# Optimization experiments

Hardware: AMD Instinct MI355X
Metric: run time of the kernel (lower is better)

Reference implementation:

```python
import jax, jax.numpy as jnp
import numpy as np

MIN_CONTEXT_SIZE = 64
FUTURE_STEPS = 12


def setup_inputs() -> dict:
    key = jax.random.key(0)
    k1, k2, k3 = jax.random.split(key, 3)
    B, T, E, C = 32, 256, 256, 256
    embeddings = jax.random.normal(k1, (B, T, E), dtype=jnp.float32)
    contexts = jax.random.normal(k2, (B, T, C), dtype=jnp.float32)
    # Bilinear comparator weight, scaled like a typical linear init
    W = jax.random.normal(k3, (E, C), dtype=jnp.float32) * (1.0 / np.sqrt(E).astype(np.float32))
    return {"embeddings": embeddings, "contexts": contexts, "W": W}


def reference(embeddings, contexts, W):
    B, T, E = embeddings.shape
    log_probs = []
    for step in range(FUTURE_STEPS):
        emb = embeddings[:, MIN_CONTEXT_SIZE + step:T]          # (B, S, E)
        ctx = contexts[:, MIN_CONTEXT_SIZE - 1:T - step - 1]    # (B, S, C)
        S = T - step - MIN_CONTEXT_SIZE
        # all-pairs bilinear scores: score[b,s,j,t] = emb[b,s] @ W @ ctx[j,t]
        proj = jnp.einsum('bse,ec->bsc', emb, W)                # (B, S, C)
        scores = jnp.einsum('bsc,jtc->bsjt', proj, ctx)         # (B, S, B, S)
        flat = scores.reshape(B * S, B * S)
        positives = jnp.diagonal(flat).reshape(B, S)            # matched (b,s) pairs
        lse = jax.nn.logsumexp(scores.reshape(B, S, B * S), axis=-1)
        lse = lse - jnp.log(jnp.asarray(B * S, dtype=scores.dtype))
        log_probs.append((positives - lse).reshape(-1))
    flat_log_probs = jnp.concatenate(log_probs, axis=0)
    return -flat_log_probs.mean()
```

## Files before the change

kernel.cpp:

```cpp
#include <hip/hip_runtime.h>
#include <hip/hip_bf16.h>
#include <math.h>


#define NROW 6144
#define TAIL0 181
#define NTERMS 71616.0f
#define LOG2E 1.44269504088896340736f
#define SHIFT2 92.33248261689366f

typedef __attribute__((ext_vector_type(8))) short short8;
typedef __attribute__((ext_vector_type(4))) float f32x4;

__device__ __forceinline__ ushort f2bf(float f) {
  union { float f; uint32_t u; } v; v.f = f;
  uint32_t u = v.u;
  return (ushort)((u + 0x7FFFu + ((u >> 16) & 1u)) >> 16);
}
__device__ __forceinline__ float expsh(float x) {
  return exp2f(fmaf(x, LOG2E, -SHIFT2));
}

__device__ __forceinline__ void gload16(const ushort* g, ushort* l) {
  __builtin_amdgcn_global_load_lds((const __attribute__((address_space(1))) void*)g,
                                   (__attribute__((address_space(3))) void*)l, 16, 0, 0);
}

__global__ __launch_bounds__(256) void k_cast(const float* __restrict__ ctx,
                                              const float* __restrict__ W,
                                              ushort* __restrict__ X,
                                              ushort* __restrict__ Wt,
                                              float* __restrict__ zbase) {
  int bi = blockIdx.x;
  if (bi < 1536) {
    int idx = bi * 256 + threadIdx.x;
    int row = idx >> 6, f4 = idx & 63;
    int j = row & 31, t = row >> 5;
    float4 f = *(const float4*)(ctx + ((size_t)(j * 256 + 63 + t)) * 256 + f4 * 4);
    ushort4 o;
    o.x = f2bf(f.x); o.y = f2bf(f.y); o.z = f2bf(f.z); o.w = f2bf(f.w);
    ((ushort4*)(X + (size_t)row * 256))[f4] = o;
  } else if (bi < 1792) {
    int c = bi - 1536, e = threadIdx.x;
    Wt[c * 256 + e] = f2bf(W[e * 256 + c]);
  } else {
    int idx = (bi - 1792) * 256 + threadIdx.x;
    if (idx < 6146) zbase[idx] = 0.f;
  }
}

__global__ __launch_bounds__(256) void k_proj(const float* __restrict__ emb,
                                              const ushort* __restrict__ Wt,
                                              ushort* __restrict__ P) {
  __shared__ ushort Al[16 * 256];
  int tid = threadIdx.x;
  int rt = blockIdx.x;
  int half = blockIdx.y;
#pragma unroll
  for (int q = 0; q < 4; ++q) {
    int cc = tid + q * 256;
    int rw = cc >> 6, f4 = cc & 63;
    int u = rt * 16 + rw, b = u / 192, urow = u - b * 192;
    float4 f = *(const float4*)(emb + ((size_t)(b * 256 + 64 + urow)) * 256 + f4 * 4);
    ushort4 o;
    o.x = f2bf(f.x); o.y = f2bf(f.y); o.z = f2bf(f.z); o.w = f2bf(f.w);
    int c8 = f4 >> 1;
    *(ushort4*)&Al[rw * 256 + ((c8 ^ (rw & 7)) * 8) + (f4 & 1) * 4] = o;
  }
  __syncthreads();

  int w = tid >> 6, l = tid & 63;
  int fr = l & 15, kb = l >> 4;
  short8 af[8];
#pragma unroll
  for (int kk = 0; kk < 8; ++kk) {
    int c8 = kk * 4 + kb;
    af[kk] = *(const short8*)&Al[fr * 256 + (c8 ^ (fr & 7)) * 8];
  }
#pragma unroll
  for (int i = 0; i < 2; ++i) {
    int ct = half * 8 + w * 2 + i;
    const short8* bp = (const short8*)(Wt + (size_t)(ct * 16 + fr) * 256);
    f32x4 acc = {0.f, 0.f, 0.f, 0.f};
#pragma unroll
    for (int kk = 0; kk < 8; ++kk)
      acc = __builtin_amdgcn_mfma_f32_16x16x32_bf16(af[kk], bp[kk * 4 + kb], acc, 0, 0, 0);
#pragma unroll
    for (int r = 0; r < 4; ++r)
      P[(size_t)(rt * 16 + kb * 4 + r) * 256 + ct * 16 + fr] = f2bf(acc[r]);
  }
}

__global__ __launch_bounds__(1024, 8) void k_scores(const ushort* __restrict__ P,
                                                    const ushort* __restrict__ X,
                                                    float* __restrict__ sum0,
                                                    float* __restrict__ tail,
                                                    float* __restrict__ pos) {
  __shared__ ushort Albuf[2][128 * 64];
  __shared__ ushort Blbuf[2][128 * 64];
  int tid = threadIdx.x;
  int w = tid >> 6, l = tid & 63;
  int wr = w >> 2, wc = w & 3;
  int rowbase = blockIdx.x * 128;
  int colbase = blockIdx.y * 128;

  int fr = l & 15, kb = l >> 4;

  int r0 = tid >> 3;
  int srcc = (tid & 7) ^ (r0 & 7);
  const ushort* gA = P + (size_t)(rowbase + r0) * 256 + srcc * 8;
  const ushort* gB = X + (size_t)(colbase + r0) * 256 + srcc * 8;

  f32x4 acc[2][2];
#pragma unroll
  for (int m = 0; m < 2; ++m)
#pragma unroll
    for (int n = 0; n < 2; ++n) acc[m][n] = {0.f, 0.f, 0.f, 0.f};

  gload16(gA, &Albuf[0][(size_t)(w * 64) * 8]);
  gload16(gB, &Blbuf[0][(size_t)(w * 64) * 8]);
  __syncthreads();

  for (int kk = 0; kk < 4; ++kk) {
    int cur = kk & 1;
    if (kk < 3) {
      int kbase = (kk + 1) * 64;
      gload16(gA + kbase, &Albuf[cur ^ 1][(size_t)(w * 64) * 8]);
      gload16(gB + kbase, &Blbuf[cur ^ 1][(size_t)(w * 64) * 8]);
    }
#pragma unroll
    for (int ks = 0; ks < 2; ++ks) {
      int sl = (ks * 4 + kb) ^ (fr & 7);
      short8 af[2], bf[2];
#pragma unroll
      for (int m = 0; m < 2; ++m)
        af[m] = *(const short8*)&Albuf[cur][((wr * 32 + m * 16 + fr) * 8 + sl) * 8];
#pragma unroll
      for (int n = 0; n < 2; ++n)
        bf[n] = *(const short8*)&Blbuf[cur][((wc * 32 + n * 16 + fr) * 8 + sl) * 8];
#pragma unroll
      for (int m = 0; m < 2; ++m)
#pragma unroll
        for (int n = 0; n < 2; ++n)
          acc[m][n] = __builtin_amdgcn_mfma_f32_16x16x32_bf16(af[m], bf[n],
                                                              acc[m][n], 0, 0, 0);
    }
    __syncthreads();
  }

  int t = blockIdx.y * 4 + wc;
#pragma unroll
  for (int m = 0; m < 2; ++m) {
    int rowg = rowbase + wr * 32 + m * 16 + kb * 4;
#pragma unroll
    for (int r = 0; r < 4; ++r) {
      int u = rowg + r;
      int b = u / 192;
      int urow = u - b * 192;
      int dt = urow - t;
      if (dt >= 0 && dt < 12) {
#pragma unroll
        for (int n = 0; n < 2; ++n) {
          int j = (wc * 32 + n * 16 + fr) & 31;
          if (j == b) pos[u * 12 + dt] = acc[m][n][r];
        }
      }
      float v = expsh(acc[m][0][r]) + expsh(acc[m][1][r]);
      v += __shfl_xor(v, 1); v += __shfl_xor(v, 2);
      v += __shfl_xor(v, 4); v += __shfl_xor(v, 8);
      if (fr == 0) {
        if (t < TAIL0) atomicAdd(&sum0[u], v);
        else tail[(size_t)(t - TAIL0) * NROW + u] = v;
      }
    }
  }
}

__global__ void k_loss(const float* __restrict__ sum0, const float* __restrict__ tail,
                       const float* __restrict__ pos, float* acc,
                       unsigned int* cnt, float* __restrict__ out) {
  int u = blockIdx.x * 256 + threadIdx.x;
  int urow = u % 192;
  int smax = urow < 11 ? urow : 11;
  float denom = sum0[u];
  float local = 0.f;
  for (int s = 11; s >= 0; --s) {
    if (s < 11) denom += tail[(size_t)(10 - s) * NROW + u];
    if (s <= smax)
      local += pos[u * 12 + s] - 64.f - __logf(denom) + __logf(32.f * (float)(192 - s));
  }
  float v = local;
  v += __shfl_xor(v, 1);  v += __shfl_xor(v, 2);  v += __shfl_xor(v, 4);
  v += __shfl_xor(v, 8);  v += __shfl_xor(v, 16); v += __shfl_xor(v, 32);
  __shared__ float red[4];
  if ((threadIdx.x & 63) == 0) red[threadIdx.x >> 6] = v;
  __syncthreads();
  if (threadIdx.x == 0) {
    atomicAdd(acc, red[0] + red[1] + red[2] + red[3]);
    __threadfence();
    unsigned int old = atomicAdd(cnt, 1u);
    if (old == 23u) {
      float tot = atomicAdd(acc, 0.0f);
      out[0] = -tot * (1.0f / NTERMS);
    }
  }
}

extern "C" void kernel_launch(void* const* d_in, const int* in_sizes, int n_in,
                              void* d_out, int out_size, void* d_ws, size_t ws_size,
                              hipStream_t stream) {
  const float* emb = (const float*)d_in[0];
  const float* ctx = (const float*)d_in[1];
  const float* W   = (const float*)d_in[2];
  char* ws = (char*)d_ws;
  ushort* P    = (ushort*)(ws + 0);
  ushort* X    = (ushort*)(ws + 3145728);
  ushort* Wt   = (ushort*)(ws + 6291456);
  float*  sum0 = (float*)(ws + 6422528);
  float*  acc  = (float*)(ws + 6447104);
  unsigned int* cnt = (unsigned int*)(ws + 6447108);
  float*  tail = (float*)(ws + 6447360);
  float*  pos  = (float*)(ws + 6717696);

  k_cast<<<1817, 256, 0, stream>>>(ctx, W, X, Wt, sum0);
  k_proj<<<dim3(384, 2), 256, 0, stream>>>(emb, Wt, P);
  k_scores<<<dim3(48, 48), 1024, 0, stream>>>(P, X, sum0, tail, pos);
  k_loss<<<24, 256, 0, stream>>>(sum0, tail, pos, acc, cnt, (float*)d_out);
}
```

Before: 67.14 us.

## Replace score-row atomics with per-block partial sums and merge cast into projection

The scores kernel no longer issues global atomicAdds per row for the non-tail columns. Each block now reduces its column-group contributions in shared memory and writes one partial per row-tile into a [46 x NROW] buffer, which the loss kernel sums. The ctx-to-bf16 cast moves from the W-transpose kernel into the projection kernel's grid, so the first kernel becomes tiny and only the W transpose sits ahead of the projection. This trades atomic contention for an extra shared-memory sync, a larger partial buffer and more reads in the loss kernel.

```diff
diff --git a/kernel.cpp b/kernel.cpp
--- a/kernel.cpp
+++ b/kernel.cpp
@@ -26,36 +26,39 @@
                                    (__attribute__((address_space(3))) void*)l, 16, 0, 0);
 }
 
-__global__ __launch_bounds__(256) void k_cast(const float* __restrict__ ctx,
-                                              const float* __restrict__ W,
-                                              ushort* __restrict__ X,
-                                              ushort* __restrict__ Wt,
-                                              float* __restrict__ zbase) {
+__global__ __launch_bounds__(256) void k_castW(const float* __restrict__ W,
+                                               ushort* __restrict__ Wt,
+                                               float* __restrict__ zbase) {
   int bi = blockIdx.x;
+  if (bi < 256) {
+    int c = bi, e = threadIdx.x;
+    Wt[c * 256 + e] = f2bf(W[e * 256 + c]);
+  } else {
+    if (threadIdx.x < 2) zbase[threadIdx.x] = 0.f;
+  }
+}
+
+__global__ __launch_bounds__(256) void k_projX(const float* __restrict__ emb,
+                                               const float* __restrict__ ctx,
+                                               const ushort* __restrict__ Wt,
+                                               ushort* __restrict__ X,
+                                               ushort* __restrict__ P) {
+  __shared__ ushort Al[16 * 256];
+  int bi = blockIdx.x;
+  int tid = threadIdx.x;
   if (bi < 1536) {
-    int idx = bi * 256 + threadIdx.x;
+    int idx = bi * 256 + tid;
     int row = idx >> 6, f4 = idx & 63;
     int j = row & 31, t = row >> 5;
     float4 f = *(const float4*)(ctx + ((size_t)(j * 256 + 63 + t)) * 256 + f4 * 4);
     ushort4 o;
     o.x = f2bf(f.x); o.y = f2bf(f.y); o.z = f2bf(f.z); o.w = f2bf(f.w);
     ((ushort4*)(X + (size_t)row * 256))[f4] = o;
-  } else if (bi < 1792) {
-    int c = bi - 1536, e = threadIdx.x;
-    Wt[c * 256 + e] = f2bf(W[e * 256 + c]);
-  } else {
-    int idx = (bi - 1792) * 256 + threadIdx.x;
-    if (idx < 6146) zbase[idx] = 0.f;
-  }
-}
-
-__global__ __launch_bounds__(256) void k_proj(const float* __restrict__ emb,
-                                              const ushort* __restrict__ Wt,
-                                              ushort* __restrict__ P) {
-  __shared__ ushort Al[16 * 256];
-  int tid = threadIdx.x;
-  int rt = blockIdx.x;
-  int half = blockIdx.y;
+    return;
+  }
+  int pb = bi - 1536;
+  int half = pb >= 384 ? 1 : 0;
+  int rt = pb - half * 384;
 #pragma unroll
   for (int q = 0; q < 4; ++q) {
     int cc = tid + q * 256;
@@ -93,7 +96,7 @@
 
 __global__ __launch_bounds__(1024, 8) void k_scores(const ushort* __restrict__ P,
                                                     const ushort* __restrict__ X,
-                                                    float* __restrict__ sum0,
+                                                    float* __restrict__ partial,
                                                     float* __restrict__ tail,
                                                     float* __restrict__ pos) {
   __shared__ ushort Albuf[2][128 * 64];
@@ -148,7 +151,9 @@
     __syncthreads();
   }
 
-  int t = blockIdx.y * 4 + wc;
+  int by = blockIdx.y;
+  int t = by * 4 + wc;
+  float* red = (float*)&Albuf[0][0];
 #pragma unroll
   for (int m = 0; m < 2; ++m) {
     int rowg = rowbase + wr * 32 + m * 16 + kb * 4;
@@ -169,20 +174,29 @@
       v += __shfl_xor(v, 1); v += __shfl_xor(v, 2);
       v += __shfl_xor(v, 4); v += __shfl_xor(v, 8);
       if (fr == 0) {
-        if (t < TAIL0) atomicAdd(&sum0[u], v);
+        if (t < TAIL0) red[(wc * 4 + wr) * 32 + (m * 16 + kb * 4 + r)] = v;
         else tail[(size_t)(t - TAIL0) * NROW + u] = v;
       }
     }
   }
-}
-
-__global__ void k_loss(const float* __restrict__ sum0, const float* __restrict__ tail,
+  __syncthreads();
+  int nb0 = TAIL0 - by * 4;
+  nb0 = nb0 > 4 ? 4 : nb0;
+  if (wc == 0 && nb0 > 0 && l < 32) {
+    float s = 0.f;
+    for (int c = 0; c < nb0; ++c) s += red[(c * 4 + wr) * 32 + l];
+    partial[(size_t)by * NROW + rowbase + wr * 32 + l] = s;
+  }
+}
+
+__global__ void k_loss(const float* __restrict__ partial, const float* __restrict__ tail,
                        const float* __restrict__ pos, float* acc,
                        unsigned int* cnt, float* __restrict__ out) {
   int u = blockIdx.x * 256 + threadIdx.x;
   int urow = u % 192;
   int smax = urow < 11 ? urow : 11;
-  float denom = sum0[u];
+  float denom = 0.f;
+  for (int g = 0; g < 46; ++g) denom += partial[(size_t)g * NROW + u];
   float local = 0.f;
   for (int s = 11; s >= 0; --s) {
     if (s < 11) denom += tail[(size_t)(10 - s) * NROW + u];
@@ -216,14 +230,14 @@
   ushort* P    = (ushort*)(ws + 0);
   ushort* X    = (ushort*)(ws + 3145728);
   ushort* Wt   = (ushort*)(ws + 6291456);
-  float*  sum0 = (float*)(ws + 6422528);
-  float*  acc  = (float*)(ws + 6447104);
-  unsigned int* cnt = (unsigned int*)(ws + 6447108);
-  float*  tail = (float*)(ws + 6447360);
-  float*  pos  = (float*)(ws + 6717696);
-
-  k_cast<<<1817, 256, 0, stream>>>(ctx, W, X, Wt, sum0);
-  k_proj<<<dim3(384, 2), 256, 0, stream>>>(emb, Wt, P);
-  k_scores<<<dim3(48, 48), 1024, 0, stream>>>(P, X, sum0, tail, pos);
-  k_loss<<<24, 256, 0, stream>>>(sum0, tail, pos, acc, cnt, (float*)d_out);
-}
+  float*  acc  = (float*)(ws + 6422528);
+  unsigned int* cnt = (unsigned int*)(ws + 6422532);
+  float*  tail = (float*)(ws + 6422784);
+  float*  pos  = (float*)(ws + 6693120);
+  float*  partial = (float*)(ws + 6988032);
+
+  k_castW<<<257, 256, 0, stream>>>(W, Wt, acc);
+  k_projX<<<2304, 256, 0, stream>>>(emb, ctx, Wt, X, P);
+  k_scores<<<dim3(48, 48), 1024, 0, stream>>>(P, X, partial, tail, pos);
+  k_loss<<<24, 256, 0, stream>>>(partial, tail, pos, acc, cnt, (float*)d_out);
+}
```

Result: slower. 84.22 us (+25.4%).
